# Performance work log

Hardware: AMD Instinct MI355X
Metric: run time of the kernel (lower is better)

The kernel has to match this reference:

```python
import jax, jax.numpy as jnp
import numpy as np

N = 50000
E = 800000
IN_DIM = 128
HID = 32
HEADS = 8
OUT_DIM = 64
OUT_CLASSES = 2
NEG_SLOPE = 0.01  # torch F.leaky_relu default


def _leaky(x):
    return jax.nn.leaky_relu(x, NEG_SLOPE)


def _seg_softmax(logits, seg, n):
    # softmax over edges grouped by destination node (DGL mailbox softmax)
    m = jax.ops.segment_max(logits, seg, num_segments=n)
    m = jnp.where(jnp.isfinite(m), m, 0.0)  # empty segments -> -inf guard
    ex = jnp.exp(logits - m[seg])
    den = jax.ops.segment_sum(ex, seg, num_segments=n)
    return ex / jnp.maximum(den[seg], 1e-12)


def _gat_layer(h, gate, src, dst, fc, a_src, a_dst):
    # fc: [H, in, out]; a_src/a_dst: [H, out] (split of attn_fc weight over the concat)
    n = h.shape[0]
    z = jnp.einsum('ni,hio->nho', h, fc)            # [N,H,O]
    zs = z[src]                                      # [E,H,O] gather over edges
    e = _leaky(jnp.einsum('eho,ho->eh', zs, a_src)
               + jnp.einsum('eho,ho->eh', z[dst], a_dst))  # [E,H]
    alpha = _seg_softmax(e * gate, dst, n)           # gate: [E,1] broadcast
    out = jax.ops.segment_sum(alpha[..., None] * zs, dst, num_segments=n)  # [N,H,O]
    return out.reshape(n, -1)                        # head concat


def setup_inputs() -> dict:
    key = jax.random.key(0)
    ks = jax.random.split(key, 16)
    h = jax.random.normal(ks[0], (N, IN_DIM), dtype=jnp.float32)
    src = jax.random.randint(ks[1], (E,), 0, N)
    dst = jax.random.randint(ks[2], (E,), 0, N)
    def lin(k, fan_in, shape):
        return jax.random.normal(k, shape, dtype=jnp.float32) / np.sqrt(fan_in)
    return {
        'h': h, 'src': src, 'dst': dst,
        # MLPPredictor (gate): W1 in->16, W2 32->8, W3 8->1
        'W1': lin(ks[3], IN_DIM, (IN_DIM, 16)), 'b1': jnp.zeros((16,), jnp.float32),
        'W2': lin(ks[4], 32, (32, 8)),          'b2': jnp.zeros((8,), jnp.float32),
        'W3': lin(ks[5], 8, (8, 1)),            'b3': jnp.zeros((1,), jnp.float32),
        # layer1: HEADS independent GateGATLayers (stacked)
        'fc1': lin(ks[6], IN_DIM, (HEADS, IN_DIM, HID)),
        'a1_src': lin(ks[7], 2 * HID, (HEADS, HID)),
        'a1_dst': lin(ks[8], 2 * HID, (HEADS, HID)),
        # layer2: single head, in = HEADS*HID -> OUT_DIM
        'fc2': lin(ks[9], HEADS * HID, (1, HEADS * HID, OUT_DIM)),
        'a2_src': lin(ks[10], 2 * OUT_DIM, (1, OUT_DIM)),
        'a2_dst': lin(ks[11], 2 * OUT_DIM, (1, OUT_DIM)),
        # MLPEdgePredictor: 2*OUT_DIM -> OUT_CLASSES
        'Wp': lin(ks[12], 2 * OUT_DIM, (2 * OUT_DIM, OUT_CLASSES)),
        'bp': jnp.zeros((OUT_CLASSES,), jnp.float32),
    }


def reference(h, src, dst, W1, b1, W2, b2, W3, b3,
              fc1, a1_src, a1_dst, fc2, a2_src, a2_dst, Wp, bp):
    # --- layer0: MLPPredictor gate (detached + min-max normalized in original) ---
    h1 = h @ W1 + b1                                   # [N,16]
    cat = jnp.concatenate([h1[src], h1[dst]], axis=1)  # [E,32]
    s = jnp.maximum(cat @ W2 + b2, 0.0) @ W3 + b3      # [E,1]
    gate = (s - s.min()) / (s.max() - s.min())         # [E,1] in [0,1]
    gate = jax.lax.stop_gradient(gate)                 # original detaches to numpy
    # --- layer1: multi-head gated GAT, leaky_relu, then single-head layer ---
    hA = _leaky(_gat_layer(h, gate, src, dst, fc1, a1_src, a1_dst))   # [N, HEADS*HID]
    hB = _gat_layer(hA, gate, src, dst, fc2, a2_src, a2_dst)          # [N, OUT_DIM]
    # --- MLPEdgePredictor ---
    edge_score = jnp.concatenate([hB[src], hB[dst]], axis=1) @ Wp + bp  # [E, OUT_CLASSES]
    return edge_score, gate
```

## Files before the change

kernel.cpp:

```cpp
#include <hip/hip_runtime.h>
#include <math.h>

#define FINF __builtin_inff()

using short8  = __attribute__((ext_vector_type(8))) short;
using floatx4 = __attribute__((ext_vector_type(4))) float;
union U4 { uint4 u; short8 s; };

__device__ __forceinline__ float leaky(float x){ return x > 0.f ? x : 0.01f*x; }

__device__ __forceinline__ unsigned int f2bf(float f){
  unsigned int x = __float_as_uint(f);
  x += 0x7FFFu + ((x >> 16) & 1u);
  return x >> 16;
}
__device__ __forceinline__ unsigned int pack2(float lo, float hi){
  return f2bf(lo) | (f2bf(hi) << 16);
}
__device__ __forceinline__ float bflo(unsigned int u){ return __uint_as_float(u << 16); }
__device__ __forceinline__ float bfhi(unsigned int u){ return __uint_as_float(u & 0xFFFF0000u); }

__global__ void k_init(int* counts8, int M){
  int i = blockIdx.x*blockDim.x + threadIdx.x;
  if (i < M) counts8[i] = 0;
}

__global__ __launch_bounds__(256) void k_h1u(const float* __restrict__ h,
        const float* __restrict__ W1, const float* __restrict__ b1,
        const float* __restrict__ W2,
        float* __restrict__ u_s, float* __restrict__ u_d, int N){
  __shared__ float lh[16][132];
  __shared__ float lw[128][16];
  __shared__ float lh1[16][17];
  int t = threadIdx.x;
  int n0 = blockIdx.x*16;
  const float4* w4 = (const float4*)W1;
  ((float4*)&lw[0][0])[t]       = w4[t];
  ((float4*)&lw[0][0])[t + 256] = w4[t + 256];
  const float4* h4 = (const float4*)(h + (size_t)n0*128);
  {
    int idx = t, row = idx >> 5, c4 = idx & 31;
    *(float4*)&lh[row][c4*4] = (n0+row < N) ? h4[idx] : make_float4(0,0,0,0);
    idx = t + 256; row = idx >> 5; c4 = idx & 31;
    *(float4*)&lh[row][c4*4] = (n0+row < N) ? h4[idx] : make_float4(0,0,0,0);
  }
  __syncthreads();
  int nl = t >> 4, j = t & 15;
  float s = b1[j];
  #pragma unroll 8
  for (int k = 0; k < 128; k++) s += lh[nl][k]*lw[k][j];
  lh1[nl][j] = s;
  __syncthreads();
  int n = n0 + nl;
  if (n < N){
    float acc = 0.f;
    if (j < 8){
      #pragma unroll
      for (int k = 0; k < 16; k++) acc += lh1[nl][k]*W2[k*8 + j];
      u_s[(size_t)n*8 + j] = acc;
    } else {
      int jj = j - 8;
      #pragma unroll
      for (int k = 0; k < 16; k++) acc += lh1[nl][k]*W2[(16 + k)*8 + jj];
      u_d[(size_t)n*8 + jj] = acc;
    }
  }
}

__global__ void k_wpack(const float* __restrict__ fc1, const float* __restrict__ fc2,
                        unsigned short* __restrict__ wp1, unsigned short* __restrict__ wp2){
  int idx = blockIdx.x*256 + threadIdx.x;
  if (idx < 32768){
    int i  = idx & 7;
    int l  = (idx >> 3) & 63;
    int kk = (idx >> 9) & 3;
    int nt = idx >> 11;
    int n = nt*16 + (l & 15);
    int k = kk*32 + ((l >> 4) << 3) + i;
    wp1[idx] = (unsigned short)f2bf(fc1[(size_t)(n >> 5)*4096 + k*32 + (n & 31)]);
  } else if (idx < 49152){
    int j = idx - 32768;
    int i  = j & 7;
    int l  = (j >> 3) & 63;
    int kk = (j >> 9) & 7;
    int nt = j >> 12;
    int n = nt*16 + (l & 15);
    int k = kk*32 + ((l >> 4) << 3) + i;
    wp2[j] = (unsigned short)f2bf(fc2[(size_t)k*64 + n]);
  }
}

__global__ __launch_bounds__(256) void k_z1m(const float* __restrict__ h,
        const unsigned short* __restrict__ wp1, unsigned short* __restrict__ z1u,
        int N){
  __shared__ uint4 lw[4096];
  int t = threadIdx.x;
  const uint4* wp4 = (const uint4*)wp1;
  #pragma unroll
  for (int i = 0; i < 16; i++) lw[t + i*256] = wp4[t + i*256];
  __syncthreads();
  int l = t & 63, wv = t >> 6;
  int n0 = blockIdx.x*64, m0 = wv*16;
  int rowA = min(n0 + m0 + (l & 15), N-1);
  const float* hr = h + (size_t)rowA*128 + ((l >> 4) << 3);
  U4 a[4];
  #pragma unroll
  for (int kk = 0; kk < 4; kk++){
    float4 f0 = *(const float4*)(hr + kk*32);
    float4 f1 = *(const float4*)(hr + kk*32 + 4);
    a[kk].u.x = pack2(f0.x, f0.y); a[kk].u.y = pack2(f0.z, f0.w);
    a[kk].u.z = pack2(f1.x, f1.y); a[kk].u.w = pack2(f1.z, f1.w);
  }
  int node0 = n0 + m0 + ((l >> 4) << 2);
  #pragma unroll
  for (int nt = 0; nt < 16; nt++){
    floatx4 acc = {0.f, 0.f, 0.f, 0.f};
    #pragma unroll
    for (int kk = 0; kk < 4; kk++){
      U4 b; b.u = lw[(nt*4 + kk)*64 + l];
      acc = __builtin_amdgcn_mfma_f32_16x16x32_bf16(a[kk].s, b.s, acc, 0, 0, 0);
    }
    int col = nt*16 + (l & 15);
    #pragma unroll
    for (int i2 = 0; i2 < 4; i2++){
      int node = node0 + i2;
      if (node < N) z1u[(size_t)node*256 + col] = (unsigned short)f2bf(acc[i2]);
    }
  }
}

__global__ void k_es_ed1(const unsigned short* __restrict__ z1u,
                         const float* __restrict__ a1s, const float* __restrict__ a1d,
                         float* __restrict__ es1, float* __restrict__ ed1, int N){
  int i = blockIdx.x*blockDim.x + threadIdx.x;
  if (i >= N*8) return;
  int n = i >> 3, hh = i & 7;
  const uint4* zr = (const uint4*)(z1u + (size_t)n*256 + hh*32);
  const float* as = a1s + hh*32;
  const float* ad = a1d + hh*32;
  float s0 = 0.f, s1 = 0.f;
  #pragma unroll
  for (int q = 0; q < 4; q++){
    uint4 v = zr[q];
    int o = q*8;
    s0 += bflo(v.x)*as[o+0] + bfhi(v.x)*as[o+1] + bflo(v.y)*as[o+2] + bfhi(v.y)*as[o+3]
        + bflo(v.z)*as[o+4] + bfhi(v.z)*as[o+5] + bflo(v.w)*as[o+6] + bfhi(v.w)*as[o+7];
    s1 += bflo(v.x)*ad[o+0] + bfhi(v.x)*ad[o+1] + bflo(v.y)*ad[o+2] + bfhi(v.y)*ad[o+3]
        + bflo(v.z)*ad[o+4] + bfhi(v.z)*ad[o+5] + bflo(v.w)*ad[o+6] + bfhi(v.w)*ad[o+7];
  }
  es1[i] = s0; ed1[i] = s1;
}

__global__ __launch_bounds__(256) void k_gate_edge(const float* __restrict__ u_s,
        const float* __restrict__ u_d,
        const int* __restrict__ src, const int* __restrict__ dst,
        const float* __restrict__ b2, const float* __restrict__ W3,
        const float* __restrict__ b3,
        float* __restrict__ sbuf, int* __restrict__ counts8,
        int* __restrict__ rank, float2* __restrict__ pmm, int E, int N){
  __shared__ float lb2[8], lw3[8];
  __shared__ float lb3;
  __shared__ float rmin[4], rmax[4];
  int t = threadIdx.x;
  if (t < 8){ lb2[t] = b2[t]; lw3[t] = W3[t]; }
  if (t == 8) lb3 = b3[0];
  __syncthreads();
  int e = blockIdx.x*blockDim.x + t;
  float s = 0.f;
  bool valid = (e < E);
  if (valid){
    int a = src[e], b = dst[e];
    float4 us0 = ((const float4*)(u_s + (size_t)a*8))[0];
    float4 us1 = ((const float4*)(u_s + (size_t)a*8))[1];
    float4 ud0 = ((const float4*)(u_d + (size_t)b*8))[0];
    float4 ud1 = ((const float4*)(u_d + (size_t)b*8))[1];
    float tv[8] = { us0.x+ud0.x, us0.y+ud0.y, us0.z+ud0.z, us0.w+ud0.w,
                    us1.x+ud1.x, us1.y+ud1.y, us1.z+ud1.z, us1.w+ud1.w };
    s = lb3;
    #pragma unroll
    for (int j = 0; j < 8; j++) s += fmaxf(tv[j] + lb2[j], 0.f)*lw3[j];
    sbuf[e] = s;
    rank[e] = atomicAdd(&counts8[(size_t)(blockIdx.x & 7)*N + b], 1);
  }
  float vmin = valid ? s : FINF;
  float vmax = valid ? s : -FINF;
  #pragma unroll
  for (int o = 32; o > 0; o >>= 1){
    vmin = fminf(vmin, __shfl_xor(vmin, o));
    vmax = fmaxf(vmax, __shfl_xor(vmax, o));
  }
  if ((t & 63) == 0){ rmin[t >> 6] = vmin; rmax[t >> 6] = vmax; }
  __syncthreads();
  if (t == 0){
    float mn = fminf(fminf(rmin[0], rmin[1]), fminf(rmin[2], rmin[3]));
    float mx = fmaxf(fmaxf(rmax[0], rmax[1]), fmaxf(rmax[2], rmax[3]));
    pmm[blockIdx.x] = make_float2(mn, mx);
  }
}

__global__ __launch_bounds__(256) void k_scan1(const int* __restrict__ counts8,
        int* __restrict__ indptr, int* __restrict__ blockSums, int N){
  __shared__ int wsum[4];
  int t = threadIdx.x;
  int base = blockIdx.x*1024 + t*4;
  int c[4];
  #pragma unroll
  for (int i = 0; i < 4; i++) c[i] = 0;
  for (int r = 0; r < 8; r++){
    const int* cr = counts8 + (size_t)r*N;
    #pragma unroll
    for (int i = 0; i < 4; i++) if (base + i < N) c[i] += cr[base + i];
  }
  int s = c[0] + c[1] + c[2] + c[3];
  int lane = t & 63, wid = t >> 6;
  int inc = s;
  #pragma unroll
  for (int o = 1; o < 64; o <<= 1){
    int v = __shfl_up(inc, o);
    if (lane >= o) inc += v;
  }
  if (lane == 63) wsum[wid] = inc;
  __syncthreads();
  int woff = 0;
  #pragma unroll
  for (int i = 0; i < 4; i++) if (i < wid) woff += wsum[i];
  int run = woff + inc - s;
  #pragma unroll
  for (int i = 0; i < 4; i++){
    if (base + i < N) indptr[base + i] = run;
    run += c[i];
  }
  if (t == 255) blockSums[blockIdx.x] = woff + inc;
}

__global__ __launch_bounds__(64) void k_scan2(int* __restrict__ blockSums,
        int* __restrict__ indptr, int B, int N,
        const float2* __restrict__ pmm, int GB, float* __restrict__ minmax){
  int t = threadIdx.x;
  int carry = 0;
  for (int b0 = 0; b0 < B; b0 += 64){
    int idx = b0 + t;
    int v = (idx < B) ? blockSums[idx] : 0;
    int inc = v;
    #pragma unroll
    for (int o = 1; o < 64; o <<= 1){
      int u = __shfl_up(inc, o);
      if (t >= o) inc += u;
    }
    if (idx < B) blockSums[idx] = carry + inc - v;
    carry += __shfl(inc, 63);
  }
  if (t == 0) indptr[N] = carry;
  float mn = FINF, mx = -FINF;
  for (int i = t; i < GB; i += 64){
    float2 v = pmm[i];
    mn = fminf(mn, v.x);
    mx = fmaxf(mx, v.y);
  }
  #pragma unroll
  for (int o = 32; o > 0; o >>= 1){
    mn = fminf(mn, __shfl_xor(mn, o));
    mx = fmaxf(mx, __shfl_xor(mx, o));
  }
  if (t == 0){ minmax[0] = mn; minmax[1] = mx; }
}

__global__ __launch_bounds__(256) void k_scan3(int* __restrict__ indptr,
        const int* __restrict__ blockSums, const int* __restrict__ counts8,
        int* __restrict__ repoff, int N){
  int i = blockIdx.x*blockDim.x + threadIdx.x;
  if (i >= N) return;
  int v = indptr[i] + blockSums[i >> 10];
  indptr[i] = v;
  int run = v;
  for (int r = 0; r < 8; r++){
    repoff[(size_t)r*N + i] = run;
    run += counts8[(size_t)r*N + i];
  }
}

__global__ void k_scatter(const int* __restrict__ src, const int* __restrict__ dst,
                          const float* __restrict__ sbuf, const float* __restrict__ minmax,
                          const int* __restrict__ rank, const int* __restrict__ repoff,
                          float* __restrict__ gate_out, uint2* __restrict__ eg,
                          int E, int N){
  int e = blockIdx.x*blockDim.x + threadIdx.x;
  if (e >= E) return;
  float mn = minmax[0], mx = minmax[1];
  float g = (sbuf[e] - mn) / (mx - mn);
  gate_out[e] = g;
  int r = blockIdx.x & 7;
  int pos = repoff[(size_t)r*N + dst[e]] + rank[e];
  uint2 v; v.x = (unsigned int)src[e]; v.y = __float_as_uint(g);
  eg[pos] = v;
}

__global__ __launch_bounds__(256) void k_gather1f(const int* __restrict__ indptr,
        const uint2* __restrict__ eg, const float* __restrict__ es1,
        const float* __restrict__ ed1, const unsigned int* __restrict__ z1b,
        unsigned int* __restrict__ hAb, int N){
  __shared__ float lap[4][64][8];
  int t = threadIdx.x;
  int w = t >> 6, lane = t & 63;
  int n = blockIdx.x*4 + w;
  if (n >= N) return;
  int hh = lane >> 3;
  float4 ev0 = *(const float4*)(ed1 + (size_t)n*8);
  float4 ev1 = *(const float4*)(ed1 + (size_t)n*8 + 4);
  int beg = indptr[n], end = indptr[n+1];
  float4 acc = make_float4(0.f,0.f,0.f,0.f);
  float den = 0.f;
  for (int c = beg; c < end; c += 64){
    int len = min(64, end - c);
    int sv = 0;
    if (lane < len){
      uint2 v = eg[c + lane];
      sv = (int)v.x;
      float g = __uint_as_float(v.y);
      float4 e0 = *(const float4*)(es1 + (size_t)sv*8);
      float4 e1 = *(const float4*)(es1 + (size_t)sv*8 + 4);
      float4 w0, w1;
      w0.x = __expf(leaky(e0.x + ev0.x)*g);
      w0.y = __expf(leaky(e0.y + ev0.y)*g);
      w0.z = __expf(leaky(e0.z + ev0.z)*g);
      w0.w = __expf(leaky(e0.w + ev0.w)*g);
      w1.x = __expf(leaky(e1.x + ev1.x)*g);
      w1.y = __expf(leaky(e1.y + ev1.y)*g);
      w1.z = __expf(leaky(e1.z + ev1.z)*g);
      w1.w = __expf(leaky(e1.w + ev1.w)*g);
      *(float4*)&lap[w][lane][0] = w0;
      *(float4*)&lap[w][lane][4] = w1;
    }
    __builtin_amdgcn_wave_barrier();
    for (int jj = 0; jj < len; jj++){
      int a = __shfl(sv, jj);
      float wgt = lap[w][jj][hh];
      uint2 zv = *(const uint2*)(z1b + (size_t)a*128 + lane*2);
      den += wgt;
      acc.x += wgt*bflo(zv.x); acc.y += wgt*bfhi(zv.x);
      acc.z += wgt*bflo(zv.y); acc.w += wgt*bfhi(zv.y);
    }
    __builtin_amdgcn_wave_barrier();
  }
  float iv = 1.f / fmaxf(den, 1e-12f);
  uint2 o;
  o.x = pack2(leaky(acc.x*iv), leaky(acc.y*iv));
  o.y = pack2(leaky(acc.z*iv), leaky(acc.w*iv));
  *(uint2*)(hAb + (size_t)n*128 + lane*2) = o;
}

__global__ __launch_bounds__(256) void k_z2m(const unsigned short* __restrict__ hAu,
        const unsigned short* __restrict__ wp2, unsigned short* __restrict__ z2u,
        int N){
  __shared__ uint4 lw[2048];
  int t = threadIdx.x;
  const uint4* wp4 = (const uint4*)wp2;
  #pragma unroll
  for (int i = 0; i < 8; i++) lw[t + i*256] = wp4[t + i*256];
  __syncthreads();
  int l = t & 63, wv = t >> 6;
  int n0 = blockIdx.x*64, m0 = wv*16;
  int rowA = min(n0 + m0 + (l & 15), N-1);
  const unsigned short* ar = hAu + (size_t)rowA*256 + ((l >> 4) << 3);
  U4 a[8];
  #pragma unroll
  for (int kk = 0; kk < 8; kk++)
    a[kk].u = *(const uint4*)(ar + kk*32);
  int node0 = n0 + m0 + ((l >> 4) << 2);
  #pragma unroll
  for (int nt = 0; nt < 4; nt++){
    floatx4 acc = {0.f, 0.f, 0.f, 0.f};
    #pragma unroll
    for (int kk = 0; kk < 8; kk++){
      U4 b; b.u = lw[(nt*8 + kk)*64 + l];
      acc = __builtin_amdgcn_mfma_f32_16x16x32_bf16(a[kk].s, b.s, acc, 0, 0, 0);
    }
    int col = nt*16 + (l & 15);
    #pragma unroll
    for (int i2 = 0; i2 < 4; i2++){
      int node = node0 + i2;
      if (node < N) z2u[(size_t)node*64 + col] = (unsigned short)f2bf(acc[i2]);
    }
  }
}

__global__ void k_es_ed2(const unsigned short* __restrict__ z2u,
                         const float* __restrict__ a2s, const float* __restrict__ a2d,
                         float* __restrict__ es2, float* __restrict__ ed2, int N){
  int n = blockIdx.x*blockDim.x + threadIdx.x;
  if (n >= N) return;
  const uint4* zr = (const uint4*)(z2u + (size_t)n*64);
  float s0 = 0.f, s1 = 0.f;
  #pragma unroll
  for (int q = 0; q < 8; q++){
    uint4 v = zr[q];
    int o = q*8;
    s0 += bflo(v.x)*a2s[o+0] + bfhi(v.x)*a2s[o+1] + bflo(v.y)*a2s[o+2] + bfhi(v.y)*a2s[o+3]
        + bflo(v.z)*a2s[o+4] + bfhi(v.z)*a2s[o+5] + bflo(v.w)*a2s[o+6] + bfhi(v.w)*a2s[o+7];
    s1 += bflo(v.x)*a2d[o+0] + bfhi(v.x)*a2d[o+1] + bflo(v.y)*a2d[o+2] + bfhi(v.y)*a2d[o+3]
        + bflo(v.z)*a2d[o+4] + bfhi(v.z)*a2d[o+5] + bflo(v.w)*a2d[o+6] + bfhi(v.w)*a2d[o+7];
  }
  es2[n] = s0; ed2[n] = s1;
}

__global__ __launch_bounds__(256) void k_gather2f(const int* __restrict__ indptr,
        const uint2* __restrict__ eg, const float* __restrict__ es2,
        const float* __restrict__ ed2, const unsigned int* __restrict__ z2b,
        const float* __restrict__ Wp, float* __restrict__ ps, float* __restrict__ pd,
        int N){
  __shared__ float lwp[256];
  int t = threadIdx.x;
  lwp[t] = Wp[t];
  __syncthreads();
  int n = blockIdx.x*8 + (t >> 5);
  if (n >= N) return;
  int l = t & 31;
  int sb = t & 32;
  float ed = ed2[n];
  int beg = indptr[n], end = indptr[n+1];
  float a0 = 0.f, a1 = 0.f, den = 0.f;
  for (int c = beg; c < end; c += 32){
    int len = min(32, end - c);
    int sv = 0; float wr = 0.f;
    if (l < len){
      uint2 v = eg[c + l];
      sv = (int)v.x;
      wr = __expf(leaky(es2[sv] + ed) * __uint_as_float(v.y));
    }
    for (int jj = 0; jj < len; jj++){
      int a = __shfl(sv, sb + jj);
      float wgt = __shfl(wr, sb + jj);
      unsigned int u = z2b[(size_t)a*32 + l];
      den += wgt;
      a0 += wgt*bflo(u);
      a1 += wgt*bfhi(u);
    }
  }
  float iv = 1.f / fmaxf(den, 1e-12f);
  float h0 = a0*iv, h1 = a1*iv;
  float s0 = h0*lwp[4*l+0] + h1*lwp[4*l+2];
  float s1 = h0*lwp[4*l+1] + h1*lwp[4*l+3];
  float d0 = h0*lwp[128+4*l+0] + h1*lwp[128+4*l+2];
  float d1 = h0*lwp[128+4*l+1] + h1*lwp[128+4*l+3];
  #pragma unroll
  for (int o = 1; o < 32; o <<= 1){
    s0 += __shfl_xor(s0, o); s1 += __shfl_xor(s1, o);
    d0 += __shfl_xor(d0, o); d1 += __shfl_xor(d1, o);
  }
  if (l == 0){
    ps[(size_t)n*2]   = s0; ps[(size_t)n*2+1] = s1;
    pd[(size_t)n*2]   = d0; pd[(size_t)n*2+1] = d1;
  }
}

__global__ void k_edgepred(const int* __restrict__ src, const int* __restrict__ dst,
                           const float* __restrict__ ps, const float* __restrict__ pd,
                           const float* __restrict__ bp, float* __restrict__ out, int E){
  int e = blockIdx.x*blockDim.x + threadIdx.x;
  if (e >= E) return;
  int a = src[e], b = dst[e];
  float2 vs = ((const float2*)ps)[a];
  float2 vd = ((const float2*)pd)[b];
  float2 o;
  o.x = vs.x + vd.x + bp[0];
  o.y = vs.y + vd.y + bp[1];
  ((float2*)out)[e] = o;
}

extern "C" void kernel_launch(void* const* d_in, const int* in_sizes, int n_in,
                              void* d_out, int out_size, void* d_ws, size_t ws_size,
                              hipStream_t stream) {
  const float* h   = (const float*)d_in[0];
  const int*   src = (const int*)d_in[1];
  const int*   dst = (const int*)d_in[2];
  const float* W1  = (const float*)d_in[3];
  const float* b1  = (const float*)d_in[4];
  const float* W2  = (const float*)d_in[5];
  const float* b2  = (const float*)d_in[6];
  const float* W3  = (const float*)d_in[7];
  const float* b3  = (const float*)d_in[8];
  const float* fc1 = (const float*)d_in[9];
  const float* a1s = (const float*)d_in[10];
  const float* a1d = (const float*)d_in[11];
  const float* fc2 = (const float*)d_in[12];
  const float* a2s = (const float*)d_in[13];
  const float* a2d = (const float*)d_in[14];
  const float* Wp  = (const float*)d_in[15];
  const float* bp  = (const float*)d_in[16];

  const int N = in_sizes[0] / 128;
  const int E = in_sizes[1];

  float* out_score = (float*)d_out;
  float* gate      = out_score + (size_t)E*2;

  char* w = (char*)d_ws;
  size_t off = 0;
  auto alloc = [&](size_t bytes) -> void* {
    off = (off + 255) & ~(size_t)255;
    void* p = w + off; off += bytes; return p;
  };
  float* u_s  = (float*)alloc((size_t)N*8*4);
  float* u_d  = (float*)alloc((size_t)N*8*4);
  unsigned short* z1u = (unsigned short*)alloc((size_t)N*256*2);
  float* es1  = (float*)alloc((size_t)N*8*4);
  float* ed1  = (float*)alloc((size_t)N*8*4);
  float* sbuf = (float*)alloc((size_t)E*4);
  unsigned short* hAu = (unsigned short*)alloc((size_t)N*256*2);
  float* es2  = (float*)alloc((size_t)N*4);
  float* ed2  = (float*)alloc((size_t)N*4);
  float* minmax = (float*)alloc(2*4);
  int* counts8 = (int*)alloc((size_t)N*8*4);
  int* repoff  = (int*)alloc((size_t)N*8*4);
  int* rank    = (int*)alloc((size_t)E*4);
  int* indptr = (int*)alloc(((size_t)N+1)*4);
  int* blockSums = (int*)alloc(1024*4);
  const int GATE_B = (E + 255)/256;
  float2* pmm = (float2*)alloc((size_t)GATE_B*8);
  uint2* eg   = (uint2*)alloc((size_t)E*8);
  unsigned short* wp1 = (unsigned short*)alloc(32768*2);
  unsigned short* wp2 = (unsigned short*)alloc(16384*2);
  (void)ws_size; (void)n_in; (void)out_size;

  unsigned short* z2u = z1u;
  float* ps  = u_s;
  float* pd  = u_d;

  const int SCAN_B = (N + 1023)/1024;

  k_init<<<(N*8 + 255)/256, 256, 0, stream>>>(counts8, N*8);
  k_h1u<<<(N + 15)/16, 256, 0, stream>>>(h, W1, b1, W2, u_s, u_d, N);
  k_wpack<<<192, 256, 0, stream>>>(fc1, fc2, wp1, wp2);
  k_z1m<<<(N + 63)/64, 256, 0, stream>>>(h, wp1, z1u, N);
  k_es_ed1<<<(N*8 + 255)/256, 256, 0, stream>>>(z1u, a1s, a1d, es1, ed1, N);
  k_gate_edge<<<GATE_B, 256, 0, stream>>>(u_s, u_d, src, dst, b2, W3, b3,
                                          sbuf, counts8, rank, pmm, E, N);
  k_scan1<<<SCAN_B, 256, 0, stream>>>(counts8, indptr, blockSums, N);
  k_scan2<<<1, 64, 0, stream>>>(blockSums, indptr, SCAN_B, N, pmm, GATE_B, minmax);
  k_scan3<<<(N + 255)/256, 256, 0, stream>>>(indptr, blockSums, counts8, repoff, N);
  k_scatter<<<GATE_B, 256, 0, stream>>>(src, dst, sbuf, minmax, rank, repoff,
                                        gate, eg, E, N);
  k_gather1f<<<(N + 3)/4, 256, 0, stream>>>(indptr, eg, es1, ed1,
                                            (const unsigned int*)z1u,
                                            (unsigned int*)hAu, N);
  k_z2m<<<(N + 63)/64, 256, 0, stream>>>(hAu, wp2, z2u, N);
  k_es_ed2<<<(N + 255)/256, 256, 0, stream>>>(z2u, a2s, a2d, es2, ed2, N);
  k_gather2f<<<(N + 7)/8, 256, 0, stream>>>(indptr, eg, es2, ed2,
                                            (const unsigned int*)z2u,
                                            Wp, ps, pd, N);
  k_edgepred<<<(E + 255)/256, 256, 0, stream>>>(src, dst, ps, pd, bp, out_score, E);
}
```

Measured before the change: 261.3 us.

## Fold attention and gate projections into MFMA GEMMs via precomposed weights

Precomposes fc·a_src/a_dst and W1·W2 into extra weight columns so the attention logits and gate node projections come out of the existing MFMA GEMM kernels as extra output tiles. This removes the separate es/ed and h1u kernels, along with their re-reads of z1/z2 and h. Weight packing, bias and counter init are merged into one prep kernel, which cuts the launch count. The logits are now computed from bf16-rounded inputs and composed weights rather than fp32 dots over the rounded z, which changes numerics slightly. The extra weight tiles are read from global memory instead of LDS.

New measurement: 228.7 us. 12.5% less time.

```diff
diff --git a/kernel.cpp b/kernel.cpp
--- a/kernel.cpp
+++ b/kernel.cpp
@@ -20,78 +20,92 @@
 __device__ __forceinline__ float bflo(unsigned int u){ return __uint_as_float(u << 16); }
 __device__ __forceinline__ float bfhi(unsigned int u){ return __uint_as_float(u & 0xFFFF0000u); }
 
-__global__ void k_init(int* counts8, int M){
-  int i = blockIdx.x*blockDim.x + threadIdx.x;
-  if (i < M) counts8[i] = 0;
-}
-
-__global__ __launch_bounds__(256) void k_h1u(const float* __restrict__ h,
-        const float* __restrict__ W1, const float* __restrict__ b1,
-        const float* __restrict__ W2,
-        float* __restrict__ u_s, float* __restrict__ u_d, int N){
-  __shared__ float lh[16][132];
-  __shared__ float lw[128][16];
-  __shared__ float lh1[16][17];
-  int t = threadIdx.x;
-  int n0 = blockIdx.x*16;
-  const float4* w4 = (const float4*)W1;
-  ((float4*)&lw[0][0])[t]       = w4[t];
-  ((float4*)&lw[0][0])[t + 256] = w4[t + 256];
-  const float4* h4 = (const float4*)(h + (size_t)n0*128);
-  {
-    int idx = t, row = idx >> 5, c4 = idx & 31;
-    *(float4*)&lh[row][c4*4] = (n0+row < N) ? h4[idx] : make_float4(0,0,0,0);
-    idx = t + 256; row = idx >> 5; c4 = idx & 31;
-    *(float4*)&lh[row][c4*4] = (n0+row < N) ? h4[idx] : make_float4(0,0,0,0);
-  }
-  __syncthreads();
-  int nl = t >> 4, j = t & 15;
-  float s = b1[j];
-  #pragma unroll 8
-  for (int k = 0; k < 128; k++) s += lh[nl][k]*lw[k][j];
-  lh1[nl][j] = s;
-  __syncthreads();
-  int n = n0 + nl;
-  if (n < N){
-    float acc = 0.f;
-    if (j < 8){
+__global__ __launch_bounds__(256) void k_prep(const float* __restrict__ fc1,
+        const float* __restrict__ fc2, const float* __restrict__ W1,
+        const float* __restrict__ W2, const float* __restrict__ b1,
+        const float* __restrict__ a1s, const float* __restrict__ a1d,
+        const float* __restrict__ a2s, const float* __restrict__ a2d,
+        unsigned short* __restrict__ wp1, unsigned short* __restrict__ wp2,
+        float* __restrict__ ubias, int* __restrict__ counts8, int N){
+  int b = blockIdx.x, t = threadIdx.x;
+  if (b < 224){
+    int idx = b*256 + t;
+    if (idx < 32768){
+      int i  = idx & 7;
+      int l  = (idx >> 3) & 63;
+      int kk = (idx >> 9) & 3;
+      int nt = idx >> 11;
+      int n = nt*16 + (l & 15);
+      int k = kk*32 + ((l >> 4) << 3) + i;
+      wp1[idx] = (unsigned short)f2bf(fc1[(size_t)(n >> 5)*4096 + k*32 + (n & 31)]);
+    } else if (idx < 34816){
+      int j = idx - 32768;
+      int i = j & 7, l = (j >> 3) & 63, kk = j >> 9;
+      int k = kk*32 + ((l >> 4) << 3) + i;
+      int c = l & 15, hh = c >> 1;
+      const float* f = fc1 + (size_t)hh*4096 + (size_t)k*32;
+      const float* av = (c & 1) ? (a1d + hh*32) : (a1s + hh*32);
+      float s = 0.f;
       #pragma unroll
-      for (int k = 0; k < 16; k++) acc += lh1[nl][k]*W2[k*8 + j];
-      u_s[(size_t)n*8 + j] = acc;
+      for (int o = 0; o < 32; o++) s += f[o]*av[o];
+      wp1[idx] = (unsigned short)f2bf(s);
+    } else if (idx < 36864){
+      int j = idx - 34816;
+      int i = j & 7, l = (j >> 3) & 63, kk = j >> 9;
+      int k = kk*32 + ((l >> 4) << 3) + i;
+      int c = l & 15;
+      float s = 0.f;
+      if (c < 8){
+        #pragma unroll
+        for (int o = 0; o < 16; o++) s += W1[k*16 + o]*W2[o*8 + c];
+      } else {
+        #pragma unroll
+        for (int o = 0; o < 16; o++) s += W1[k*16 + o]*W2[(16 + o)*8 + (c - 8)];
+      }
+      wp1[idx] = (unsigned short)f2bf(s);
     } else {
-      int jj = j - 8;
-      #pragma unroll
-      for (int k = 0; k < 16; k++) acc += lh1[nl][k]*W2[(16 + k)*8 + jj];
-      u_d[(size_t)n*8 + jj] = acc;
-    }
-  }
-}
-
-__global__ void k_wpack(const float* __restrict__ fc1, const float* __restrict__ fc2,
-                        unsigned short* __restrict__ wp1, unsigned short* __restrict__ wp2){
-  int idx = blockIdx.x*256 + threadIdx.x;
-  if (idx < 32768){
-    int i  = idx & 7;
-    int l  = (idx >> 3) & 63;
-    int kk = (idx >> 9) & 3;
-    int nt = idx >> 11;
-    int n = nt*16 + (l & 15);
-    int k = kk*32 + ((l >> 4) << 3) + i;
-    wp1[idx] = (unsigned short)f2bf(fc1[(size_t)(n >> 5)*4096 + k*32 + (n & 31)]);
-  } else if (idx < 49152){
-    int j = idx - 32768;
-    int i  = j & 7;
-    int l  = (j >> 3) & 63;
-    int kk = (j >> 9) & 7;
-    int nt = j >> 12;
-    int n = nt*16 + (l & 15);
-    int k = kk*32 + ((l >> 4) << 3) + i;
-    wp2[j] = (unsigned short)f2bf(fc2[(size_t)k*64 + n]);
+      int j = idx - 36864;
+      if (j < 16384){
+        int i  = j & 7, l = (j >> 3) & 63, kk = (j >> 9) & 7, nt = j >> 12;
+        int n = nt*16 + (l & 15);
+        int k = kk*32 + ((l >> 4) << 3) + i;
+        wp2[j] = (unsigned short)f2bf(fc2[(size_t)k*64 + n]);
+      } else {
+        int q = j - 16384;
+        int i = q & 7, l = (q >> 3) & 63, kk = q >> 9;
+        int k = kk*32 + ((l >> 4) << 3) + i;
+        int c = l & 15;
+        float s = 0.f;
+        if (c == 0){
+          for (int o = 0; o < 64; o++) s += fc2[(size_t)k*64 + o]*a2s[o];
+        } else if (c == 1){
+          for (int o = 0; o < 64; o++) s += fc2[(size_t)k*64 + o]*a2d[o];
+        }
+        wp2[j] = (unsigned short)f2bf(s);
+      }
+    }
+  } else if (b == 224){
+    if (t < 16){
+      float s = 0.f;
+      if (t < 8){
+        #pragma unroll
+        for (int o = 0; o < 16; o++) s += b1[o]*W2[o*8 + t];
+      } else {
+        #pragma unroll
+        for (int o = 0; o < 16; o++) s += b1[o]*W2[(16 + o)*8 + (t - 8)];
+      }
+      ubias[t] = s;
+    }
+  } else {
+    int i = (b - 225)*256 + t;
+    if (i < N*8) counts8[i] = 0;
   }
 }
 
 __global__ __launch_bounds__(256) void k_z1m(const float* __restrict__ h,
-        const unsigned short* __restrict__ wp1, unsigned short* __restrict__ z1u,
+        const unsigned short* __restrict__ wp1, const float* __restrict__ ubias,
+        unsigned short* __restrict__ z1u, float* __restrict__ es1,
+        float* __restrict__ ed1, float* __restrict__ u_s, float* __restrict__ u_d,
         int N){
   __shared__ uint4 lw[4096];
   int t = threadIdx.x;
@@ -112,43 +126,47 @@
     a[kk].u.z = pack2(f1.x, f1.y); a[kk].u.w = pack2(f1.z, f1.w);
   }
   int node0 = n0 + m0 + ((l >> 4) << 2);
-  #pragma unroll
-  for (int nt = 0; nt < 16; nt++){
-    floatx4 acc = {0.f, 0.f, 0.f, 0.f};
+  int c = l & 15;
+  float ub = ubias[c];
+  #pragma unroll
+  for (int nt = 0; nt < 18; nt++){
+    floatx4 acc;
+    float b0 = (nt == 17) ? ub : 0.f;
+    acc[0] = b0; acc[1] = b0; acc[2] = b0; acc[3] = b0;
     #pragma unroll
     for (int kk = 0; kk < 4; kk++){
-      U4 b; b.u = lw[(nt*4 + kk)*64 + l];
-      acc = __builtin_amdgcn_mfma_f32_16x16x32_bf16(a[kk].s, b.s, acc, 0, 0, 0);
-    }
-    int col = nt*16 + (l & 15);
-    #pragma unroll
-    for (int i2 = 0; i2 < 4; i2++){
-      int node = node0 + i2;
-      if (node < N) z1u[(size_t)node*256 + col] = (unsigned short)f2bf(acc[i2]);
-    }
-  }
-}
-
-__global__ void k_es_ed1(const unsigned short* __restrict__ z1u,
-                         const float* __restrict__ a1s, const float* __restrict__ a1d,
-                         float* __restrict__ es1, float* __restrict__ ed1, int N){
-  int i = blockIdx.x*blockDim.x + threadIdx.x;
-  if (i >= N*8) return;
-  int n = i >> 3, hh = i & 7;
-  const uint4* zr = (const uint4*)(z1u + (size_t)n*256 + hh*32);
-  const float* as = a1s + hh*32;
-  const float* ad = a1d + hh*32;
-  float s0 = 0.f, s1 = 0.f;
-  #pragma unroll
-  for (int q = 0; q < 4; q++){
-    uint4 v = zr[q];
-    int o = q*8;
-    s0 += bflo(v.x)*as[o+0] + bfhi(v.x)*as[o+1] + bflo(v.y)*as[o+2] + bfhi(v.y)*as[o+3]
-        + bflo(v.z)*as[o+4] + bfhi(v.z)*as[o+5] + bflo(v.w)*as[o+6] + bfhi(v.w)*as[o+7];
-    s1 += bflo(v.x)*ad[o+0] + bfhi(v.x)*ad[o+1] + bflo(v.y)*ad[o+2] + bfhi(v.y)*ad[o+3]
-        + bflo(v.z)*ad[o+4] + bfhi(v.z)*ad[o+5] + bflo(v.w)*ad[o+6] + bfhi(v.w)*ad[o+7];
-  }
-  es1[i] = s0; ed1[i] = s1;
+      U4 bfr;
+      bfr.u = (nt < 16) ? lw[(nt*4 + kk)*64 + l] : wp4[(nt*4 + kk)*64 + l];
+      acc = __builtin_amdgcn_mfma_f32_16x16x32_bf16(a[kk].s, bfr.s, acc, 0, 0, 0);
+    }
+    if (nt < 16){
+      int col = nt*16 + c;
+      #pragma unroll
+      for (int i2 = 0; i2 < 4; i2++){
+        int node = node0 + i2;
+        if (node < N) z1u[(size_t)node*256 + col] = (unsigned short)f2bf(acc[i2]);
+      }
+    } else if (nt == 16){
+      int hh = c >> 1;
+      #pragma unroll
+      for (int i2 = 0; i2 < 4; i2++){
+        int node = node0 + i2;
+        if (node < N){
+          if (c & 1) ed1[node*8 + hh] = acc[i2];
+          else       es1[node*8 + hh] = acc[i2];
+        }
+      }
+    } else {
+      #pragma unroll
+      for (int i2 = 0; i2 < 4; i2++){
+        int node = node0 + i2;
+        if (node < N){
+          if (c < 8) u_s[(size_t)node*8 + c] = acc[i2];
+          else       u_d[(size_t)node*8 + (c - 8)] = acc[i2];
+        }
+      }
+    }
+  }
 }
 
 __global__ __launch_bounds__(256) void k_gate_edge(const float* __restrict__ u_s,
@@ -351,7 +369,7 @@
 
 __global__ __launch_bounds__(256) void k_z2m(const unsigned short* __restrict__ hAu,
         const unsigned short* __restrict__ wp2, unsigned short* __restrict__ z2u,
-        int N){
+        float* __restrict__ es2, float* __restrict__ ed2, int N){
   __shared__ uint4 lw[2048];
   int t = threadIdx.x;
   const uint4* wp4 = (const uint4*)wp2;
@@ -367,40 +385,34 @@
   for (int kk = 0; kk < 8; kk++)
     a[kk].u = *(const uint4*)(ar + kk*32);
   int node0 = n0 + m0 + ((l >> 4) << 2);
-  #pragma unroll
-  for (int nt = 0; nt < 4; nt++){
+  int c = l & 15;
+  #pragma unroll
+  for (int nt = 0; nt < 5; nt++){
     floatx4 acc = {0.f, 0.f, 0.f, 0.f};
     #pragma unroll
     for (int kk = 0; kk < 8; kk++){
-      U4 b; b.u = lw[(nt*8 + kk)*64 + l];
-      acc = __builtin_amdgcn_mfma_f32_16x16x32_bf16(a[kk].s, b.s, acc, 0, 0, 0);
-    }
-    int col = nt*16 + (l & 15);
-    #pragma unroll
-    for (int i2 = 0; i2 < 4; i2++){
-      int node = node0 + i2;
-      if (node < N) z2u[(size_t)node*64 + col] = (unsigned short)f2bf(acc[i2]);
-    }
-  }
-}
-
-__global__ void k_es_ed2(const unsigned short* __restrict__ z2u,
-                         const float* __restrict__ a2s, const float* __restrict__ a2d,
-                         float* __restrict__ es2, float* __restrict__ ed2, int N){
-  int n = blockIdx.x*blockDim.x + threadIdx.x;
-  if (n >= N) return;
-  const uint4* zr = (const uint4*)(z2u + (size_t)n*64);
-  float s0 = 0.f, s1 = 0.f;
-  #pragma unroll
-  for (int q = 0; q < 8; q++){
-    uint4 v = zr[q];
-    int o = q*8;
-    s0 += bflo(v.x)*a2s[o+0] + bfhi(v.x)*a2s[o+1] + bflo(v.y)*a2s[o+2] + bfhi(v.y)*a2s[o+3]
-        + bflo(v.z)*a2s[o+4] + bfhi(v.z)*a2s[o+5] + bflo(v.w)*a2s[o+6] + bfhi(v.w)*a2s[o+7];
-    s1 += bflo(v.x)*a2d[o+0] + bfhi(v.x)*a2d[o+1] + bflo(v.y)*a2d[o+2] + bfhi(v.y)*a2d[o+3]
-        + bflo(v.z)*a2d[o+4] + bfhi(v.z)*a2d[o+5] + bflo(v.w)*a2d[o+6] + bfhi(v.w)*a2d[o+7];
-  }
-  es2[n] = s0; ed2[n] = s1;
+      U4 bfr;
+      bfr.u = (nt < 4) ? lw[(nt*8 + kk)*64 + l] : wp4[(nt*8 + kk)*64 + l];
+      acc = __builtin_amdgcn_mfma_f32_16x16x32_bf16(a[kk].s, bfr.s, acc, 0, 0, 0);
+    }
+    if (nt < 4){
+      int col = nt*16 + c;
+      #pragma unroll
+      for (int i2 = 0; i2 < 4; i2++){
+        int node = node0 + i2;
+        if (node < N) z2u[(size_t)node*64 + col] = (unsigned short)f2bf(acc[i2]);
+      }
+    } else {
+      #pragma unroll
+      for (int i2 = 0; i2 < 4; i2++){
+        int node = node0 + i2;
+        if (node < N){
+          if (c == 0) es2[node] = acc[i2];
+          else if (c == 1) ed2[node] = acc[i2];
+        }
+      }
+    }
+  }
 }
 
 __global__ __launch_bounds__(256) void k_gather2f(const int* __restrict__ indptr,
@@ -510,6 +522,7 @@
   float* es2  = (float*)alloc((size_t)N*4);
   float* ed2  = (float*)alloc((size_t)N*4);
   float* minmax = (float*)alloc(2*4);
+  float* ubias  = (float*)alloc(16*4);
   int* counts8 = (int*)alloc((size_t)N*8*4);
   int* repoff  = (int*)alloc((size_t)N*8*4);
   int* rank    = (int*)alloc((size_t)E*4);
@@ -518,8 +531,8 @@
   const int GATE_B = (E + 255)/256;
   float2* pmm = (float2*)alloc((size_t)GATE_B*8);
   uint2* eg   = (uint2*)alloc((size_t)E*8);
-  unsigned short* wp1 = (unsigned short*)alloc(32768*2);
-  unsigned short* wp2 = (unsigned short*)alloc(16384*2);
+  unsigned short* wp1 = (unsigned short*)alloc(36864*2);
+  unsigned short* wp2 = (unsigned short*)alloc(20480*2);
   (void)ws_size; (void)n_in; (void)out_size;
 
   unsigned short* z2u = z1u;
@@ -527,12 +540,11 @@
   float* pd  = u_d;
 
   const int SCAN_B = (N + 1023)/1024;
-
-  k_init<<<(N*8 + 255)/256, 256, 0, stream>>>(counts8, N*8);
-  k_h1u<<<(N + 15)/16, 256, 0, stream>>>(h, W1, b1, W2, u_s, u_d, N);
-  k_wpack<<<192, 256, 0, stream>>>(fc1, fc2, wp1, wp2);
-  k_z1m<<<(N + 63)/64, 256, 0, stream>>>(h, wp1, z1u, N);
-  k_es_ed1<<<(N*8 + 255)/256, 256, 0, stream>>>(z1u, a1s, a1d, es1, ed1, N);
+  const int INIT_B = (N*8 + 255)/256;
+
+  k_prep<<<225 + INIT_B, 256, 0, stream>>>(fc1, fc2, W1, W2, b1, a1s, a1d,
+                                           a2s, a2d, wp1, wp2, ubias, counts8, N);
+  k_z1m<<<(N + 63)/64, 256, 0, stream>>>(h, wp1, ubias, z1u, es1, ed1, u_s, u_d, N);
   k_gate_edge<<<GATE_B, 256, 0, stream>>>(u_s, u_d, src, dst, b2, W3, b3,
                                           sbuf, counts8, rank, pmm, E, N);
   k_scan1<<<SCAN_B, 256, 0, stream>>>(counts8, indptr, blockSums, N);
@@ -543,8 +555,7 @@
   k_gather1f<<<(N + 3)/4, 256, 0, stream>>>(indptr, eg, es1, ed1,
                                             (const unsigned int*)z1u,
                                             (unsigned int*)hAu, N);
-  k_z2m<<<(N + 63)/64, 256, 0, stream>>>(hAu, wp2, z2u, N);
-  k_es_ed2<<<(N + 255)/256, 256, 0, stream>>>(z2u, a2s, a2d, es2, ed2, N);
+  k_z2m<<<(N + 63)/64, 256, 0, stream>>>(hAu, wp2, z2u, es2, ed2, N);
   k_gather2f<<<(N + 7)/8, 256, 0, stream>>>(indptr, eg, es2, ed2,
                                             (const unsigned int*)z2u,
                                             Wp, ps, pd, N);
```
